# Performance work log

Hardware: AMD Instinct MI355X
Metric: run time of the kernel (lower is better)

## Reference

```python
import jax, jax.numpy as jnp
import numpy as np

EPS = 1e-8

def setup_inputs() -> dict:
    key = jax.random.key(0)
    k1, k2 = jax.random.split(key)
    x = jax.random.normal(k1, (16, 64, 256, 256), dtype=jnp.float32)
    mask = jax.random.uniform(k2, (16, 1, 256, 256), dtype=jnp.float32)
    return {"x": x, "mask": mask}

def _masked_stats(x, w):
    # x: [B,C,H,W], w: [B,1,H,W] in {0,1}. Returns mean, unbiased std: [B,C,1,1]
    n = jnp.sum(w, axis=(2, 3), keepdims=True)          # [B,1,1,1]
    mu = jnp.sum(x * w, axis=(2, 3), keepdims=True) / n  # [B,C,1,1]
    # two-pass unbiased variance (matches torch.std with ddof=1)
    var = jnp.sum(w * (x - mu) ** 2, axis=(2, 3), keepdims=True) / (n - 1.0)
    return mu, jnp.sqrt(var)

def reference(x, mask):
    fg = mask >= 0.5                      # [B,1,H,W] bool
    fgf = fg.astype(x.dtype)
    bgf = 1.0 - fgf
    mu_fg, sig_fg = _masked_stats(x, fgf)
    mu_bg, sig_bg = _masked_stats(x, bgf)
    harmonized = (x - mu_bg) / (sig_bg + EPS) * sig_fg + mu_fg
    return jnp.where(fg, x, harmonized)
```

## Files before the change

### kernel.cpp

```cpp
#include <hip/hip_runtime.h>


#define HW    65536
#define HW4   16384
#define C     64
#define B     16
#define NSLICE (B * C)
#define TOTAL4 (NSLICE * HW4)

__global__ __launch_bounds__(512) void stats_kernel(
    const float* __restrict__ x, const float* __restrict__ mask,
    float4* __restrict__ stats) {
  const int slice = blockIdx.x;
  const int b = slice >> 6;
  const float4* __restrict__ x4 = (const float4*)(x + (size_t)slice * HW);
  const float4* __restrict__ m4 = (const float4*)(mask + (size_t)b * HW);

  float cnt = 0.f, sf = 0.f, s2f = 0.f, st = 0.f, s2t = 0.f;

#pragma unroll 4
  for (int i = threadIdx.x; i < HW4; i += 512) {
    float4 xv = x4[i];
    float4 mv = m4[i];
    const float* xe = (const float*)&xv;
    const float* me = (const float*)&mv;
#pragma unroll
    for (int k = 0; k < 4; ++k) {
      float xk = xe[k];
      float x2 = xk * xk;
      bool fg = me[k] >= 0.5f;
      st  += xk;
      s2t += x2;
      cnt += fg ? 1.f : 0.f;
      sf  += fg ? xk : 0.f;
      s2f += fg ? x2 : 0.f;
    }
  }

#pragma unroll
  for (int off = 32; off > 0; off >>= 1) {
    cnt += __shfl_down(cnt, off);
    sf  += __shfl_down(sf,  off);
    s2f += __shfl_down(s2f, off);
    st  += __shfl_down(st,  off);
    s2t += __shfl_down(s2t, off);
  }

  __shared__ float red[8][5];
  const int wave = threadIdx.x >> 6;
  const int lane = threadIdx.x & 63;
  if (lane == 0) {
    red[wave][0] = cnt; red[wave][1] = sf; red[wave][2] = s2f;
    red[wave][3] = st;  red[wave][4] = s2t;
  }
  __syncthreads();

  if (threadIdx.x == 0) {
    float tcnt = 0.f, tsf = 0.f, ts2f = 0.f, tst = 0.f, ts2t = 0.f;
#pragma unroll
    for (int w = 0; w < 8; ++w) {
      tcnt += red[w][0]; tsf += red[w][1]; ts2f += red[w][2];
      tst  += red[w][3]; ts2t += red[w][4];
    }
    float n_fg = tcnt;
    float n_bg = (float)HW - tcnt;
    float s_bg  = tst  - tsf;
    float s2_bg = ts2t - ts2f;

    float mu_fg  = tsf / fmaxf(n_fg, 1.f);
    float var_fg = fmaxf((ts2f - n_fg * mu_fg * mu_fg) / fmaxf(n_fg - 1.f, 1.f), 0.f);
    float sig_fg = sqrtf(var_fg);

    float mu_bg  = s_bg / fmaxf(n_bg, 1.f);
    float var_bg = fmaxf((s2_bg - n_bg * mu_bg * mu_bg) / fmaxf(n_bg - 1.f, 1.f), 0.f);
    float sig_bg = sqrtf(var_bg);

    float A = sig_fg / (sig_bg + 1e-8f);
    stats[slice] = make_float4(A, mu_bg, mu_fg, 0.f);
  }
}

__global__ __launch_bounds__(256) void apply_kernel(
    const float* __restrict__ x, const float* __restrict__ mask,
    const float4* __restrict__ stats, float* __restrict__ out) {
  const float4* __restrict__ x4 = (const float4*)x;
  const float4* __restrict__ m4 = (const float4*)mask;
  float4* __restrict__ o4 = (float4*)out;

  const int stride = gridDim.x * blockDim.x;
  for (int i = blockIdx.x * blockDim.x + threadIdx.x; i < TOTAL4; i += stride) {
    const int slice = i >> 14;
    const int b = slice >> 6;
    const int in_slice = i & (HW4 - 1);
    float4 stv = stats[slice];
    float4 xv = x4[i];
    float4 mv = m4[(b << 14) + in_slice];
    float4 ov;
    float* oe = (float*)&ov;
    const float* xe = (const float*)&xv;
    const float* me = (const float*)&mv;
#pragma unroll
    for (int k = 0; k < 4; ++k) {
      float xk = xe[k];
      float h = fmaf(xk - stv.y, stv.x, stv.z);
      oe[k] = (me[k] >= 0.5f) ? xk : h;
    }
    o4[i] = ov;
  }
}

extern "C" void kernel_launch(void* const* d_in, const int* in_sizes, int n_in,
                              void* d_out, int out_size, void* d_ws, size_t ws_size,
                              hipStream_t stream) {
  const float* x = (const float*)d_in[0];
  const float* mask = (const float*)d_in[1];
  float* out = (float*)d_out;
  float4* stats = (float4*)d_ws;

  stats_kernel<<<NSLICE, 512, 0, stream>>>(x, mask, stats);
  apply_kernel<<<8192, 256, 0, stream>>>(x, mask, stats, out);
}
```

Before: 496.8 us.

## Fuse stats and apply into one register-resident kernel per slice

Merges the statistics and apply kernels into a single kernel where each 1024-thread block loads one channel slice into registers, reduces the masked statistics, then writes the harmonized output from the registers. This removes the second global read of x and the mask, and the stats workspace round trip. Foreground bits are packed into bitmasks so the mask is not reloaded. Block-to-slice mapping is swizzled across XCDs so slices sharing a mask batch sit on the same XCD. Risks: high register pressure reduces occupancy, and there is no overlap between the load and store phases inside a block.

```diff
diff --git a/kernel.cpp b/kernel.cpp
--- a/kernel.cpp
+++ b/kernel.cpp
@@ -1,28 +1,33 @@
 #include <hip/hip_runtime.h>
 
 
-#define HW    65536
-#define HW4   16384
-#define C     64
-#define B     16
-#define NSLICE (B * C)
-#define TOTAL4 (NSLICE * HW4)
+#define HW     65536
+#define HW4    16384
+#define NSLICE 1024
+#define TPB    1024
+#define ITERS  16
+#define NXCD   8
 
-__global__ __launch_bounds__(512) void stats_kernel(
+__global__ __launch_bounds__(TPB) void fused_adain_kernel(
     const float* __restrict__ x, const float* __restrict__ mask,
-    float4* __restrict__ stats) {
-  const int slice = blockIdx.x;
+    float* __restrict__ out) {
+  const int slice = (blockIdx.x % NXCD) * (NSLICE / NXCD) + blockIdx.x / NXCD;
   const int b = slice >> 6;
+
   const float4* __restrict__ x4 = (const float4*)(x + (size_t)slice * HW);
   const float4* __restrict__ m4 = (const float4*)(mask + (size_t)b * HW);
+  float4* __restrict__ o4 = (float4*)(out + (size_t)slice * HW);
 
+  float4 xv[ITERS];
+  unsigned fgb[2] = {0u, 0u};
   float cnt = 0.f, sf = 0.f, s2f = 0.f, st = 0.f, s2t = 0.f;
 
-#pragma unroll 4
-  for (int i = threadIdx.x; i < HW4; i += 512) {
-    float4 xv = x4[i];
+#pragma unroll
+  for (int it = 0; it < ITERS; ++it) {
+    const int i = threadIdx.x + it * TPB;
+    xv[it] = x4[i];
     float4 mv = m4[i];
-    const float* xe = (const float*)&xv;
+    const float* xe = (const float*)&xv[it];
     const float* me = (const float*)&mv;
 #pragma unroll
     for (int k = 0; k < 4; ++k) {
@@ -34,6 +39,7 @@
       cnt += fg ? 1.f : 0.f;
       sf  += fg ? xk : 0.f;
       s2f += fg ? x2 : 0.f;
+      fgb[it >> 3] |= (unsigned)fg << ((it & 7) * 4 + k);
     }
   }
 
@@ -46,7 +52,8 @@
     s2t += __shfl_down(s2t, off);
   }
 
-  __shared__ float red[8][5];
+  __shared__ float red[16][5];
+  __shared__ float bc[3];
   const int wave = threadIdx.x >> 6;
   const int lane = threadIdx.x & 63;
   if (lane == 0) {
@@ -58,7 +65,7 @@
   if (threadIdx.x == 0) {
     float tcnt = 0.f, tsf = 0.f, ts2f = 0.f, tst = 0.f, ts2t = 0.f;
 #pragma unroll
-    for (int w = 0; w < 8; ++w) {
+    for (int w = 0; w < 16; ++w) {
       tcnt += red[w][0]; tsf += red[w][1]; ts2f += red[w][2];
       tst  += red[w][3]; ts2t += red[w][4];
     }
@@ -75,35 +82,28 @@
     float var_bg = fmaxf((s2_bg - n_bg * mu_bg * mu_bg) / fmaxf(n_bg - 1.f, 1.f), 0.f);
     float sig_bg = sqrtf(var_bg);
 
-    float A = sig_fg / (sig_bg + 1e-8f);
-    stats[slice] = make_float4(A, mu_bg, mu_fg, 0.f);
+    bc[0] = sig_fg / (sig_bg + 1e-8f);
+    bc[1] = mu_bg;
+    bc[2] = mu_fg;
   }
-}
+  __syncthreads();
 
-__global__ __launch_bounds__(256) void apply_kernel(
-    const float* __restrict__ x, const float* __restrict__ mask,
-    const float4* __restrict__ stats, float* __restrict__ out) {
-  const float4* __restrict__ x4 = (const float4*)x;
-  const float4* __restrict__ m4 = (const float4*)mask;
-  float4* __restrict__ o4 = (float4*)out;
+  const float A     = bc[0];
+  const float mu_bg = bc[1];
+  const float mu_fg = bc[2];
 
-  const int stride = gridDim.x * blockDim.x;
-  for (int i = blockIdx.x * blockDim.x + threadIdx.x; i < TOTAL4; i += stride) {
-    const int slice = i >> 14;
-    const int b = slice >> 6;
-    const int in_slice = i & (HW4 - 1);
-    float4 stv = stats[slice];
-    float4 xv = x4[i];
-    float4 mv = m4[(b << 14) + in_slice];
+#pragma unroll
+  for (int it = 0; it < ITERS; ++it) {
+    const int i = threadIdx.x + it * TPB;
     float4 ov;
     float* oe = (float*)&ov;
-    const float* xe = (const float*)&xv;
-    const float* me = (const float*)&mv;
+    const float* xe = (const float*)&xv[it];
 #pragma unroll
     for (int k = 0; k < 4; ++k) {
       float xk = xe[k];
-      float h = fmaf(xk - stv.y, stv.x, stv.z);
-      oe[k] = (me[k] >= 0.5f) ? xk : h;
+      float h = fmaf(xk - mu_bg, A, mu_fg);
+      bool fg = (fgb[it >> 3] >> ((it & 7) * 4 + k)) & 1u;
+      oe[k] = fg ? xk : h;
     }
     o4[i] = ov;
   }
@@ -115,8 +115,7 @@
   const float* x = (const float*)d_in[0];
   const float* mask = (const float*)d_in[1];
   float* out = (float*)d_out;
-  float4* stats = (float4*)d_ws;
+  (void)d_ws; (void)ws_size;
 
-  stats_kernel<<<NSLICE, 512, 0, stream>>>(x, mask, stats);
-  apply_kernel<<<8192, 256, 0, stream>>>(x, mask, stats, out);
+  fused_adain_kernel<<<NSLICE, TPB, 0, stream>>>(x, mask, out);
 }
```

New measurement: 465.4 us. -6.3%, faster.
